# Performance work log

Hardware: AMD Instinct MI355X
Metric: run time of the kernel (lower is better)

Reference implementation:

```python
import jax, jax.numpy as jnp
import numpy as np

EPS = 1e-8
TEMP = 0.1
D, H = 512, 256  # hidden_dim, hidden_dim // 2
BI, R = 64, 36   # images, regions
BC, W = 64, 50   # captions, words


def _l2norm(x):
    n = jnp.linalg.norm(x, axis=-1, keepdims=True)
    return x / jnp.maximum(n, 1e-12)


def _gate(x, w1, b1, w2, b2):
    h = jax.nn.relu(x @ w1 + b1)
    return jax.nn.sigmoid(h @ w2 + b2)  # [..., 1]


def setup_inputs() -> dict:
    key = jax.random.key(0)
    ks = jax.random.split(key, 12)
    imgs = jax.random.normal(ks[0], (BI, R, D), dtype=jnp.float32)
    caps = jax.random.normal(ks[1], (BC, W, D), dtype=jnp.float32)
    img_lens = jax.random.randint(ks[2], (BI,), 1, R + 1).at[0].set(R).astype(jnp.int32)
    cap_lens = jax.random.randint(ks[3], (BC,), 1, W + 1).at[0].set(W).astype(jnp.int32)
    s = 0.02
    return {
        'imgs': imgs, 'caps': caps,
        'soft_w1': jax.random.normal(ks[4], (D, H), dtype=jnp.float32) * s,
        'soft_b1': jnp.zeros((H,), dtype=jnp.float32),
        'soft_w2': jax.random.normal(ks[5], (H, 1), dtype=jnp.float32) * s,
        'soft_b2': jnp.zeros((1,), dtype=jnp.float32),
        'hard_w1': jax.random.normal(ks[6], (D, H), dtype=jnp.float32) * s,
        'hard_b1': jnp.zeros((H,), dtype=jnp.float32),
        'hard_w2': jax.random.normal(ks[7], (H, 1), dtype=jnp.float32) * s,
        'hard_b2': jnp.zeros((1,), dtype=jnp.float32),
        'img_lens': img_lens, 'cap_lens': cap_lens,
    }


def reference(imgs, caps, soft_w1, soft_b1, soft_w2, soft_b2,
              hard_w1, hard_b1, hard_w2, hard_b2, img_lens, cap_lens):
    Bi, R_, D_ = imgs.shape
    Bc, W_, _ = caps.shape
    img_mask = jnp.arange(R_)[None, :] < img_lens[:, None]  # [Bi,R]
    cap_mask = jnp.arange(W_)[None, :] < cap_lens[:, None]  # [Bc,W]
    mask = img_mask[:, None, :, None] & cap_mask[None, :, None, :]  # [Bi,Bc,R,W]

    # fine-grained region-word similarities
    sims = jnp.einsum('ird,cwd->icrw', imgs, caps)

    # hard (top-1) attention: argmax over words, one-hot scatter, re-masked
    idx = jnp.argmax(jnp.where(mask, sims, -1.0), axis=-1)  # [Bi,Bc,R]
    hard_attn = jnp.where(mask, jax.nn.one_hot(idx, W_, dtype=sims.dtype), 0.0)

    # soft attention with temperature and mask
    soft = jax.nn.softmax(jnp.where(mask, sims / TEMP, -jnp.inf), axis=-1)
    soft_attn = jnp.where(mask, soft, 0.0)

    hard_wc = jnp.einsum('icrw,cwd->icrd', hard_attn, caps)
    soft_wc = jnp.einsum('icrw,cwd->icrd', soft_attn, caps)

    # per-region learned gates, normalized to sum ~1
    sg = _gate(imgs, soft_w1, soft_b1, soft_w2, soft_b2)  # [Bi,R,1]
    hg = _gate(imgs, hard_w1, hard_b1, hard_w2, hard_b2)  # [Bi,R,1]
    tot = sg + hg + EPS
    sg = (sg / tot)[:, None, :, :]  # [Bi,1,R,1]
    hg = (hg / tot)[:, None, :, :]

    mixed = sg * soft_wc + hg * hard_wc  # [Bi,Bc,R,D]

    # per-pair, per-region cosine similarity
    out = jnp.einsum('ird,icrd->icr', _l2norm(imgs), _l2norm(mixed))
    return jnp.where(img_mask[:, None, :], out, -1.0)  # [Bi,Bc,R]
```

## Files before the change

kernel.cpp:

```cpp
#include <hip/hip_runtime.h>
#include <math.h>

#define BI 64
#define RR 36
#define BC 64
#define WW 50
#define DD 512
#define HH 256
#define CST 132

typedef _Float16 f16x8 __attribute__((ext_vector_type(8)));
typedef _Float16 f16x4 __attribute__((ext_vector_type(4)));
typedef float    f32x4 __attribute__((ext_vector_type(4)));
typedef float    f32x16 __attribute__((ext_vector_type(16)));

__device__ __forceinline__ float wave_sum(float v){
  #pragma unroll
  for (int off=32; off>0; off>>=1) v += __shfl_xor(v, off, 64);
  return v;
}
__device__ __forceinline__ float wave_max(float v){
  #pragma unroll
  for (int off=32; off>0; off>>=1) v = fmaxf(v, __shfl_xor(v, off, 64));
  return v;
}

__device__ __forceinline__ void gl_lds16(const _Float16* g, _Float16* l){
  __builtin_amdgcn_global_load_lds(
      (const __attribute__((address_space(1))) unsigned int*)g,
      (__attribute__((address_space(3))) unsigned int*)l, 16, 0, 0);
}

__global__ __launch_bounds__(256) void prepgram_kernel(
    const float* __restrict__ imgs, const float* __restrict__ caps,
    const float* __restrict__ sw1, const float* __restrict__ hw1,
    _Float16* __restrict__ Ah, _Float16* __restrict__ Al,
    _Float16* __restrict__ Bh, _Float16* __restrict__ Bl,
    float* __restrict__ G, _Float16* __restrict__ Gfrag)
{
  __shared__ __align__(16) float smem[64*64];
  if (blockIdx.x < 1504){
    int u = blockIdx.x*256 + threadIdx.x;
    _Float16 *dh, *dl; int idx;
    if (u < 144*1024){ idx = u;            dh = Ah; dl = Al; }
    else             { idx = u - 144*1024; dh = Bh; dl = Bl; }
    const int tile = idx >> 10, rem = idx & 1023, ks = rem >> 6, lane = rem & 63;
    const int k0 = ks*32 + (lane >> 4)*8;
    f16x8 hv, lv;
    if (u < 144*1024 || tile < 200){
      const float* src = (u < 144*1024) ? imgs : caps;
      const int m = tile*16 + (lane & 15);
      const float* p = src + (size_t)m*DD + k0;
      #pragma unroll
      for (int j=0;j<8;j++){
        float a = p[j];
        _Float16 h = (_Float16)a;
        hv[j] = h;
        lv[j] = (_Float16)((a - (float)h) * 2048.0f);
      }
    } else {
      const int n = (tile-200)*16 + (lane & 15);
      const float* src = (n < HH) ? (sw1 + n) : (hw1 + n - HH);
      #pragma unroll
      for (int j=0;j<8;j++){
        float a = src[(size_t)(k0+j)*HH];
        _Float16 h = (_Float16)a;
        hv[j] = h;
        lv[j] = (_Float16)((a - (float)h) * 2048.0f);
      }
    }
    *(f16x8*)(dh + (size_t)idx*8) = hv;
    *(f16x8*)(dl + (size_t)idx*8) = lv;
  } else {
    float* Gt = smem;
    const int c = blockIdx.x - 1504;
    const int t = threadIdx.x, lane = t & 63, wv = t >> 6;
    const int wm = wv & 1, wn = wv >> 1;
    const float* cbase = caps + (size_t)c*WW*DD;

    f32x16 P, Q;
    #pragma unroll
    for (int e=0;e<16;e++){ P[e]=0.f; Q[e]=0.f; }

    const int r  = lane & 31;
    const int k8 = (lane >> 5)*8;
    const int wA = wm*32 + r;
    const int wB = wn*32 + r;
    const float* pA = cbase + (size_t)wA*DD + k8;
    const float* pB = cbase + (size_t)wB*DD + k8;

    for (int ks=0; ks<32; ks++){
      const int k0 = ks*16;
      float4 a0, a1, b0, b1;
      if (wA < WW){ a0 = *(const float4*)(pA + k0); a1 = *(const float4*)(pA + k0 + 4); }
      else        { a0 = (float4){0,0,0,0}; a1 = a0; }
      if (wB < WW){ b0 = *(const float4*)(pB + k0); b1 = *(const float4*)(pB + k0 + 4); }
      else        { b0 = (float4){0,0,0,0}; b1 = b0; }
      float av[8] = {a0.x,a0.y,a0.z,a0.w,a1.x,a1.y,a1.z,a1.w};
      float bw[8] = {b0.x,b0.y,b0.z,b0.w,b1.x,b1.y,b1.z,b1.w};
      f16x8 ah, al, bh, bl;
      #pragma unroll
      for (int j=0;j<8;j++){
        _Float16 h = (_Float16)av[j];
        ah[j] = h; al[j] = (_Float16)((av[j]-(float)h)*2048.0f);
        _Float16 g = (_Float16)bw[j];
        bh[j] = g; bl[j] = (_Float16)((bw[j]-(float)g)*2048.0f);
      }
      P = __builtin_amdgcn_mfma_f32_32x32x16_f16(ah, bh, P,0,0,0);
      Q = __builtin_amdgcn_mfma_f32_32x32x16_f16(ah, bl, Q,0,0,0);
      Q = __builtin_amdgcn_mfma_f32_32x32x16_f16(al, bh, Q,0,0,0);
    }

    const int col = wn*32 + (lane & 31);
    #pragma unroll
    for (int reg=0; reg<16; reg++){
      const int row = wm*32 + (reg&3) + 8*(reg>>2) + 4*(lane>>5);
      float g = P[reg] + Q[reg]*(1.0f/2048.0f);
      Gt[row*64 + col] = g;
      if (row < WW && col < WW)
        G[(size_t)c*WW*WW + row*WW + col] = g;
    }
    __syncthreads();

    #pragma unroll
    for (int tile=0; tile<4; tile++){
      int flat = t*4;
      int ks2 = flat>>9, L=(flat>>3)&63, j0=flat&7;
      const bool ones = (tile==3) && ((L&15)==2);
      int n  = tile*16 + (L&15);
      int kk = ks2*32 + ((L>>4)<<3) + j0;
      f16x4 v;
      #pragma unroll
      for (int e=0;e<4;e++)
        v[e] = ones ? (_Float16)1.0f : (_Float16)Gt[n*64 + kk + e];
      *(f16x4*)&Gfrag[(size_t)c*4096 + (tile*2+ks2)*512 + L*8 + j0] = v;
    }
  }
}

__global__ __launch_bounds__(256, 2) void sgemm_hgate_kernel(
    const _Float16* __restrict__ Ah, const _Float16* __restrict__ Al,
    const _Float16* __restrict__ Bh, const _Float16* __restrict__ Bl,
    float* __restrict__ Sp,
    const float* __restrict__ imgs,
    const float* __restrict__ sb1, const float* __restrict__ hb1,
    const float* __restrict__ sw2, const float* __restrict__ hw2,
    float* __restrict__ drawS, float* __restrict__ drawH,
    float* __restrict__ rnraw)
{
  __shared__ _Float16 lds[2*16384];
  const int t = threadIdx.x, lane = t & 63, wv = t >> 6;

  if (blockIdx.x >= 36){
    const int sg  = blockIdx.x - 36;
    const int xcd = sg & 7, sidx = sg >> 3;
    const int l   = (xcd < 2 ? xcd*57 : 114 + (xcd-2)*56) + sidx;
    const int st  = l / 45, wi = l - st*45;
    const int mbg = st & 1, nbg = st >> 1;
    const int mb  = mbg*9 + wi/5;
    const int nb  = nbg*5 + wi%5;
    const int wm = wv & 1, wn = wv >> 1;

    f32x4 P[4][4], Q[4][4];
    #pragma unroll
    for (int a=0;a<4;a++)
      #pragma unroll
      for (int b=0;b<4;b++){ P[a][b]=(f32x4){0,0,0,0}; Q[a][b]=(f32x4){0,0,0,0}; }

    const _Float16* sbase = (wv==0)?Ah:(wv==1)?Al:(wv==2)?Bh:Bl;
    const size_t gtb = (size_t)((wv<2)? mb : nb)*8;
    _Float16* buf0 = lds + wv*4096;
    _Float16* buf1 = lds + 16384 + wv*4096;

    #pragma unroll
    for (int s=0;s<8;s++)
      gl_lds16(sbase + (((gtb+s)*16 + 0)*64 + lane)*8, buf0 + s*512);
    asm volatile("s_waitcnt vmcnt(0)" ::: "memory");
    __syncthreads();

    for (int ks=0; ks<16; ks++){
      if (ks < 15){
        _Float16* nb_ = ((ks+1) & 1) ? buf1 : buf0;
        #pragma unroll
        for (int s=0;s<8;s++)
          gl_lds16(sbase + (((gtb+s)*16 + (ks+1))*64 + lane)*8, nb_ + s*512);
      }

      const _Float16* L = lds + (ks & 1)*16384;
      f16x8 a_h[4], a_l[4], b_h[4], b_l[4];
      #pragma unroll
      for (int x=0;x<4;x++){
        a_h[x] = *(const f16x8*)&L[        (wm*4+x)*512 + lane*8];
        a_l[x] = *(const f16x8*)&L[ 4096 + (wm*4+x)*512 + lane*8];
        b_h[x] = *(const f16x8*)&L[ 8192 + (wn*4+x)*512 + lane*8];
        b_l[x] = *(const f16x8*)&L[12288 + (wn*4+x)*512 + lane*8];
      }
      #pragma unroll
      for (int mi=0;mi<4;mi++)
        #pragma unroll
        for (int ni=0;ni<4;ni++){
          P[mi][ni] = __builtin_amdgcn_mfma_f32_16x16x32_f16(a_h[mi], b_h[ni], P[mi][ni],0,0,0);
          Q[mi][ni] = __builtin_amdgcn_mfma_f32_16x16x32_f16(a_h[mi], b_l[ni], Q[mi][ni],0,0,0);
          Q[mi][ni] = __builtin_amdgcn_mfma_f32_16x16x32_f16(a_l[mi], b_h[ni], Q[mi][ni],0,0,0);
        }

      if (ks < 15)
        asm volatile("s_waitcnt vmcnt(0)" ::: "memory");
      __syncthreads();
    }

    const int r0 = mb*128 + wm*64 + ((lane>>4)<<2);
    const int c0 = nb*128 + wn*64 + (lane&15);
    size_t pr[16]; size_t pc[4];
    #pragma unroll
    for (int mi=0;mi<4;mi++)
      #pragma unroll
      for (int reg=0;reg<4;reg++){
        unsigned row = (unsigned)(r0 + mi*16 + reg);
        unsigned i = row / 36u, rr_ = row - i*36u;
        pr[mi*4+reg] = (size_t)i*115200u + (size_t)rr_*50u;
      }
    #pragma unroll
    for (int ni=0;ni<4;ni++){
      unsigned col = (unsigned)(c0 + ni*16);
      unsigned cc = col / 50u, w = col - cc*50u;
      pc[ni] = (size_t)cc*1800u + w;
    }
    #pragma unroll
    for (int mi=0;mi<4;mi++)
      #pragma unroll
      for (int ni=0;ni<4;ni++)
        #pragma unroll
        for (int reg=0;reg<4;reg++)
          Sp[pr[mi*4+reg] + pc[ni]] =
              P[mi][ni][reg] + Q[mi][ni][reg]*(1.0f/2048.0f);
    return;
  }

  const int mb = blockIdx.x >> 1;
  const int br = blockIdx.x & 1;
  const int wm = wv & 1, wn = wv >> 1;

  f32x4 P[4][8];
  #pragma unroll
  for (int a=0;a<4;a++)
    #pragma unroll
    for (int b=0;b<8;b++) P[a][b]=(f32x4){0,0,0,0};

  const _Float16* Bbase = Bh + (size_t)(200 + br*16)*8192;

  #pragma unroll
  for (int s=0;s<6;s++){
    const int u = wv*6 + s;
    const _Float16* src = (u < 8)
      ? (Ah    + ((size_t)((mb*8 + u)*16 + 0)*64 + lane)*8)
      : (Bbase + ((size_t)((u-8)  *16 + 0)*64 + lane)*8);
    _Float16* dst = (u < 8) ? (lds + u*512) : (lds + 4096 + (u-8)*512);
    gl_lds16(src, dst);
  }
  asm volatile("s_waitcnt vmcnt(0)" ::: "memory");
  __syncthreads();

  for (int ks=0; ks<16; ks++){
    if (ks < 15){
      _Float16* buf = lds + (((ks+1) & 1) ? 16384 : 0);
      #pragma unroll
      for (int s=0;s<6;s++){
        const int u = wv*6 + s;
        const _Float16* src = (u < 8)
          ? (Ah    + ((size_t)((mb*8 + u)*16 + (ks+1))*64 + lane)*8)
          : (Bbase + ((size_t)((u-8)  *16 + (ks+1))*64 + lane)*8);
        _Float16* dst = (u < 8) ? (buf + u*512) : (buf + 4096 + (u-8)*512);
        gl_lds16(src, dst);
      }
    }

    const _Float16* L = lds + (ks & 1)*16384;
    f16x8 a[4], b[8];
    #pragma unroll
    for (int x=0;x<4;x++)
      a[x] = *(const f16x8*)&L[(wm*4+x)*512 + lane*8];
    #pragma unroll
    for (int y=0;y<8;y++)
      b[y] = *(const f16x8*)&L[4096 + (wn*8+y)*512 + lane*8];
    #pragma unroll
    for (int mi=0;mi<4;mi++)
      #pragma unroll
      for (int ni=0;ni<8;ni++)
        P[mi][ni] = __builtin_amdgcn_mfma_f32_16x16x32_f16(a[mi], b[ni], P[mi][ni],0,0,0);

    if (ks < 15)
      asm volatile("s_waitcnt vmcnt(0)" ::: "memory");
    __syncthreads();
  }

  const float* b1 = br ? hb1 : sb1;
  const float* w2 = br ? hw2 : sw2;
  float bvv[8], wvv[8];
  #pragma unroll
  for (int ni=0;ni<8;ni++){
    const int cb = wn*128 + ni*16 + (lane&15);
    bvv[ni] = b1[cb]; wvv[ni] = w2[cb];
  }
  float contrib[16];
  #pragma unroll
  for (int mi=0;mi<4;mi++)
    #pragma unroll
    for (int reg=0;reg<4;reg++){
      float cacc = 0.f;
      #pragma unroll
      for (int ni=0;ni<8;ni++)
        cacc = fmaf(fmaxf(P[mi][ni][reg] + bvv[ni], 0.f), wvv[ni], cacc);
      #pragma unroll
      for (int off=1; off<16; off<<=1) cacc += __shfl_xor(cacc, off, 64);
      contrib[mi*4+reg] = cacc;
    }

  float* red = (float*)lds;
  if ((lane & 15) == 0){
    const int rbase = wm*64 + ((lane>>4)<<2);
    #pragma unroll
    for (int mi=0;mi<4;mi++)
      #pragma unroll
      for (int reg=0;reg<4;reg++)
        red[wn*128 + rbase + mi*16 + reg] = contrib[mi*4+reg];
  }
  __syncthreads();
  if (t < 128){
    float draw = red[t] + red[128 + t];
    (br ? drawH : drawS)[mb*128 + t] = draw;
  }

  if (br == 0){
    const int row = mb*128 + (t >> 1);
    const float* p = imgs + (size_t)row*DD + (t & 1)*256;
    float ss = 0.f;
    #pragma unroll
    for (int q=0;q<64;q++){
      float4 x = ((const float4*)p)[q];
      ss += x.x*x.x + x.y*x.y + x.z*x.z + x.w*x.w;
    }
    ss += __shfl_xor(ss, 1, 64);
    if ((t & 1) == 0) rnraw[row] = ss;
  }
}

__global__ __launch_bounds__(256) void epi_kernel(
    const float* __restrict__ Sp,
    const int* __restrict__ img_lens, const int* __restrict__ cap_lens,
    const float* __restrict__ drawS, const float* __restrict__ drawH,
    const float* __restrict__ rnraw,
    const float* __restrict__ G, const _Float16* __restrict__ Gfrag,
    const float* __restrict__ sb2, const float* __restrict__ hb2,
    float* __restrict__ out)
{
  __shared__ __align__(16) _Float16 FT[4][48*72];
  const int t = threadIdx.x, lane = t & 63;
  const int wv = __builtin_amdgcn_readfirstlane(t >> 6);
  const int pair = blockIdx.x*4 + wv;
  const int i = pair >> 6, c = pair & 63;
  const int l = lane & 15, g = lane >> 4;
  const int cap_len = cap_lens[c];
  const int img_len = img_lens[i];

  int4 gf[8];
  #pragma unroll
  for (int q=0;q<8;q++)
    gf[q] = ((const int4*)(Gfrag + (size_t)c*4096))[q*64 + lane];

  const float* sbp = Sp + (size_t)i*115200 + (size_t)c*1800;
  float sv[3][16];
  #pragma unroll
  for (int nt=0;nt<3;nt++)
    #pragma unroll
    for (int ks=0;ks<2;ks++){
      const float* p = sbp + (nt*16+l)*50 + ks*32 + g*8;
      #pragma unroll
      for (int h=0;h<4;h++){
        float2 v2 = *(const float2*)(p + h*2);
        sv[nt][ks*8 + h*2]     = v2.x;
        sv[nt][ks*8 + h*2 + 1] = v2.y;
      }
    }

  float avA[3]; int aiA[3]; float denA[3], tSA[3];
  f16x8 e16[3][2];
  #pragma unroll
  for (int nt=0;nt<3;nt++){
    float best = -INFINITY; int bw = 64;
    #pragma unroll
    for (int j=0;j<16;j++){
      int w = (j>>3)*32 + g*8 + (j&7);
      if (w < cap_len){
        float s = sv[nt][j];
        if (s > best){ best = s; bw = w; }
      }
    }
    #pragma unroll
    for (int off=16; off<64; off<<=1){
      float ov = __shfl_xor(best, off, 64);
      int   ow = __shfl_xor(bw,   off, 64);
      if (ov > best || (ov == best && ow < bw)){ best = ov; bw = ow; }
    }
    avA[nt] = best; aiA[nt] = (bw < 64) ? bw : 0;

    float dsum = 0.f, tsum = 0.f;
    #pragma unroll
    for (int ks=0;ks<2;ks++)
      #pragma unroll
      for (int j=0;j<8;j++){
        int w = ks*32 + g*8 + j;
        float s = sv[nt][ks*8+j];
        float e = (w < cap_len) ? __expf(10.0f*(s - best)) : 0.f;
        _Float16 eh = (_Float16)e;
        e16[nt][ks][j] = eh;
        dsum += (float)eh;
        tsum += (float)(_Float16)(e * s);
      }
    dsum += __shfl_xor(dsum,16,64); dsum += __shfl_xor(dsum,32,64);
    tsum += __shfl_xor(tsum,16,64); tsum += __shfl_xor(tsum,32,64);
    denA[nt] = dsum; tSA[nt] = tsum;
  }

  _Float16* ft = &FT[wv][0];
  #pragma unroll
  for (int mt=0;mt<4;mt++)
    #pragma unroll
    for (int nt=0;nt<3;nt++){
      f32x4 acc = (f32x4){0,0,0,0};
      #pragma unroll
      for (int ks=0;ks<2;ks++){
        f16x8 ga = *(const f16x8*)&gf[mt*2+ks];
        acc = __builtin_amdgcn_mfma_f32_16x16x32_f16(ga, e16[nt][ks], acc,0,0,0);
      }
      f16x4 fv;
      #pragma unroll
      for (int r2=0;r2<4;r2++) fv[r2] = (_Float16)acc[r2];
      *(f16x4*)&ft[(nt*16+l)*72 + mt*16 + g*4] = fv;
    }

  float tQA[3];
  #pragma unroll
  for (int nt=0;nt<3;nt++){
    float q = 0.f;
    #pragma unroll
    for (int ks=0;ks<2;ks++){
      f16x8 fv = *(const f16x8*)&ft[(nt*16+l)*72 + ks*32 + g*8];
      #pragma unroll
      for (int j=0;j<8;j++)
        q += (float)e16[nt][ks][j] * (float)fv[j];
    }
    q += __shfl_xor(q,16,64); q += __shfl_xor(q,32,64);
    tQA[nt] = q;
  }

  if (lane < 16){
    const float sb2v = sb2[0], hb2v = hb2[0];
    #pragma unroll
    for (int nt=0;nt<3;nt++){
      const int rr = nt*16 + lane;
      if (rr < RR){
        const int ai = aiA[nt];
        const float av = avA[nt];
        float dh = (float)ft[rr*72 + ai];
        float hh = G[(size_t)c*WW*WW + ai*(WW+1)];
        float hv = (av > -1.0f) ? 1.f : 0.f;
        const int rg = i*RR + rr;
        float sg_ = 1.f/(1.f+__expf(-(drawS[rg] + sb2v)));
        float hg_ = 1.f/(1.f+__expf(-(drawH[rg] + hb2v)));
        float tot = sg_ + hg_ + 1e-8f;
        float gs = sg_/tot, gh = hg_/tot;
        float rx = 1.f/fmaxf(sqrtf(rnraw[rg]), 1e-12f);
        float dn = (float)(_Float16)denA[nt];
        float rd = 1.f/dn;
        float num = gs*(tSA[nt]*rd) + hv*gh*av;
        float n2  = gs*gs*(tQA[nt]*rd*rd) + hv*(2.f*gs*gh*(dh*rd) + gh*gh*hh);
        float ov  = num * rx / fmaxf(sqrtf(fmaxf(n2, 0.f)), 1e-12f);
        out[((size_t)i*BC + c)*RR + rr] = (rr < img_len) ? ov : -1.0f;
      }
    }
  }
}

__global__ __launch_bounds__(256) void gates_kernel(
    const float* __restrict__ imgs,
    const float* __restrict__ sw1, const float* __restrict__ sb1,
    const float* __restrict__ sw2, const float* __restrict__ sb2,
    const float* __restrict__ hw1, const float* __restrict__ hb1,
    const float* __restrict__ hw2, const float* __restrict__ hb2,
    float* __restrict__ sgn, float* __restrict__ hgn, float* __restrict__ rn)
{
  __shared__ __align__(16) float xs[8*DD];
  __shared__ float red[16*256];
  __shared__ float nr[8];
  const int t = threadIdx.x;
  const int row0 = blockIdx.x * 8;
  if (t < 8) nr[t] = 0.f;
  __syncthreads();
  const float4* src = (const float4*)(imgs + (size_t)row0*DD);
  #pragma unroll
  for (int m=0;m<4;m++){
    int n = m*256+t;
    float4 v = src[n];
    ((float4*)xs)[n] = v;
    float ss = v.x*v.x+v.y*v.y+v.z*v.z+v.w*v.w;
    atomicAdd(&nr[n>>7], ss);
  }
  __syncthreads();
  float accS[8]={0,0,0,0,0,0,0,0};
  float accH[8]={0,0,0,0,0,0,0,0};
  for (int k=0;k<DD;k+=4){
    float a0=sw1[(k+0)*HH+t], a1=sw1[(k+1)*HH+t], a2=sw1[(k+2)*HH+t], a3=sw1[(k+3)*HH+t];
    float b0=hw1[(k+0)*HH+t], b1=hw1[(k+1)*HH+t], b2=hw1[(k+2)*HH+t], b3=hw1[(k+3)*HH+t];
    #pragma unroll
    for (int r=0;r<8;r++){
      float4 x = *(const float4*)&xs[r*DD+k];
      accS[r]=fmaf(x.x,a0,accS[r]); accS[r]=fmaf(x.y,a1,accS[r]);
      accS[r]=fmaf(x.z,a2,accS[r]); accS[r]=fmaf(x.w,a3,accS[r]);
      accH[r]=fmaf(x.x,b0,accH[r]); accH[r]=fmaf(x.y,b1,accH[r]);
      accH[r]=fmaf(x.z,b2,accH[r]); accH[r]=fmaf(x.w,b3,accH[r]);
    }
  }
  const float b1s=sb1[t], b1h=hb1[t], w2s=sw2[t], w2h=hw2[t];
  #pragma unroll
  for (int r=0;r<8;r++){
    red[r*256+t]     = w2s * fmaxf(accS[r]+b1s, 0.f);
    red[(8+r)*256+t] = w2h * fmaxf(accH[r]+b1h, 0.f);
  }
  __syncthreads();
  const int wv=t>>6, ln=t&63;
  #pragma unroll
  for (int q=0;q<4;q++){
    int rr_ = wv*4+q;
    float v = red[rr_*256+ln]+red[rr_*256+ln+64]+red[rr_*256+ln+128]+red[rr_*256+ln+192];
    v = wave_sum(v);
    if (ln==0) red[rr_*256] = v;
  }
  __syncthreads();
  if (t<8){
    float os = red[t*256] + sb2[0];
    float oh = red[(8+t)*256] + hb2[0];
    float s = 1.f/(1.f+__expf(-os));
    float h = 1.f/(1.f+__expf(-oh));
    float tot = s+h+1e-8f;
    sgn[row0+t] = s/tot;
    hgn[row0+t] = h/tot;
    rn[row0+t]  = 1.f/fmaxf(sqrtf(nr[t]), 1e-12f);
  }
}

__global__ __launch_bounds__(256) void gram_fb_kernel(
    const float* __restrict__ caps, float* __restrict__ G)
{
  __shared__ __align__(16) float cs[WW*CST];
  const int c    = blockIdx.x >> 2;
  const int tile = blockIdx.x & 3;
  const int w0   = tile*13;
  const int nw   = (tile==3) ? 11 : 13;
  const int t=threadIdx.x, lane=t&63, wv=t>>6;
  const int wl = lane < WW ? lane : WW-1;
  float acc[4]={0.f,0.f,0.f,0.f};
  for (int k0=0;k0<DD;k0+=128){
    __syncthreads();
    for (int n=t;n<WW*32;n+=256){
      int row=n>>5, c4=(n&31)*4;
      *(float4*)&cs[row*CST+c4] = *(const float4*)(caps + ((size_t)c*WW+row)*DD + k0 + c4);
    }
    __syncthreads();
    for (int k=0;k<128;k+=4){
      float4 cv = *(const float4*)&cs[wl*CST+k];
      #pragma unroll
      for (int q=0;q<4;q++){
        int lw = wv + q*4;
        if (lw < nw){
          float4 bv = *(const float4*)&cs[(w0+lw)*CST+k];
          acc[q]=fmaf(bv.x,cv.x,acc[q]); acc[q]=fmaf(bv.y,cv.y,acc[q]);
          acc[q]=fmaf(bv.z,cv.z,acc[q]); acc[q]=fmaf(bv.w,cv.w,acc[q]);
        }
      }
    }
  }
  if (lane < WW){
    #pragma unroll
    for (int q=0;q<4;q++){
      int lw = wv + q*4;
      if (lw < nw) G[(size_t)c*WW*WW + (w0+lw)*WW + lane] = acc[q];
    }
  }
}

__global__ __launch_bounds__(256) void pair_kernel(
    const float* __restrict__ imgs, const float* __restrict__ caps,
    const int* __restrict__ img_lens, const int* __restrict__ cap_lens,
    const float* __restrict__ sgn, const float* __restrict__ hgn,
    const float* __restrict__ rn,
    const float* __restrict__ G, float* __restrict__ out)
{
  __shared__ __align__(16) float smem[WW*CST + 52*52 + RR*52];
  float* cs = smem;
  float* Gs = smem + WW*CST;
  float* As = Gs + 52*52;
  const int bx = blockIdx.x;
  const int i = bx >> 6, c = bx & 63;
  const int t = threadIdx.x, lane = t&63;
  const int wv = __builtin_amdgcn_readfirstlane(t>>6);
  const int wl = lane < WW ? lane : WW-1;
  const int cap_len = cap_lens[c];
  const int img_len = img_lens[i];
  for (int n=t;n<52*52;n+=256){
    int w=n/52, w2=n-w*52;
    Gs[n] = (w<WW && w2<WW) ? G[(size_t)c*WW*WW + w*WW + w2] : 0.f;
  }
  float acc[9]={0,0,0,0,0,0,0,0,0};
  const float* ib = imgs + ((size_t)i*RR + wv*9)*DD;
  for (int k0=0;k0<DD;k0+=128){
    __syncthreads();
    for (int n=t;n<WW*32;n+=256){
      int row=n>>5, c4=(n&31)*4;
      *(float4*)&cs[row*CST+c4] = *(const float4*)(caps + ((size_t)c*WW+row)*DD + k0 + c4);
    }
    __syncthreads();
    for (int k=0;k<128;k+=4){
      float4 cv = *(const float4*)&cs[wl*CST+k];
      #pragma unroll
      for (int j=0;j<9;j++){
        float4 iv = *(const float4*)(ib + j*DD + k0 + k);
        acc[j]=fmaf(iv.x,cv.x,acc[j]); acc[j]=fmaf(iv.y,cv.y,acc[j]);
        acc[j]=fmaf(iv.z,cv.z,acc[j]); acc[j]=fmaf(iv.w,cv.w,acc[j]);
      }
    }
  }
  for (int j=0;j<9;j++){
    const int r = wv*9 + j;
    const float s = acc[j];
    float av; int ai;
    if (lane < cap_len){ av = s;     ai = lane; }
    else if (lane < WW){ av = -1.0f; ai = lane; }
    else               { av = -INFINITY; ai = 64; }
    #pragma unroll
    for (int off=32; off>0; off>>=1){
      float ov = __shfl_xor(av, off, 64);
      int   oi = __shfl_xor(ai, off, 64);
      if (ov > av || (ov == av && oi < ai)){ av = ov; ai = oi; }
    }
    float zv = (lane < cap_len) ? s*10.0f : -INFINITY;
    float zm = wave_max(zv);
    float e  = (lane < cap_len) ? __expf(zv - zm) : 0.f;
    float den = wave_sum(e);
    if (lane < 52) As[r*52 + lane] = (lane < WW) ? e : 0.f;
    float m = 0.f;
    #pragma unroll
    for (int g=0; g<13; g++){
      float4 ab = *(const float4*)&As[r*52 + g*4];
      m = fmaf(ab.x, Gs[(g*4+0)*52+wl], m);
      m = fmaf(ab.y, Gs[(g*4+1)*52+wl], m);
      m = fmaf(ab.z, Gs[(g*4+2)*52+wl], m);
      m = fmaf(ab.w, Gs[(g*4+3)*52+wl], m);
    }
    float tS = wave_sum(e * s);
    float tQ = wave_sum(e * m);
    float dh = __shfl(m, ai, 64);
    float hh = Gs[ai*52 + ai];
    float hv = (ai < cap_len) ? 1.f : 0.f;
    const int rg = i*RR + r;
    float gs = sgn[rg], gh = hgn[rg], rx = rn[rg];
    float rd = 1.f/den;
    float num = gs*(tS*rd) + hv*gh*av;
    float n2  = gs*gs*(tQ*rd*rd) + hv*(2.f*gs*gh*(dh*rd) + gh*gh*hh);
    float ov  = num * rx / fmaxf(sqrtf(fmaxf(n2, 0.f)), 1e-12f);
    if (lane==0) out[((size_t)i*BC + c)*RR + r] = (r < img_len) ? ov : -1.0f;
  }
}

extern "C" void kernel_launch(void* const* d_in, const int* in_sizes, int n_in,
                              void* d_out, int out_size, void* d_ws, size_t ws_size,
                              hipStream_t stream)
{
  const float* imgs = (const float*)d_in[0];
  const float* caps = (const float*)d_in[1];
  const float* sw1  = (const float*)d_in[2];
  const float* sb1  = (const float*)d_in[3];
  const float* sw2  = (const float*)d_in[4];
  const float* sb2  = (const float*)d_in[5];
  const float* hw1  = (const float*)d_in[6];
  const float* hb1  = (const float*)d_in[7];
  const float* hw2  = (const float*)d_in[8];
  const float* hb2  = (const float*)d_in[9];
  const int* img_lens = (const int*)d_in[10];
  const int* cap_lens = (const int*)d_in[11];

  char* base = (char*)d_ws;
  float*    drawS = (float*)(base + 0);
  float*    drawH = (float*)(base + 9216);
  float*    rnraw = (float*)(base + 18432);
  float*    G     = (float*)(base + 27648);
  _Float16* Gfrag = (_Float16*)(base + 667648);
  _Float16* Ah    = (_Float16*)(base + 1191936);
  _Float16* Al    = (_Float16*)(base + 3551232);
  _Float16* Bh    = (_Float16*)(base + 5910528);
  _Float16* Bl    = (_Float16*)(base + 9711616);
  float*    Sp    = (float*)(base + 18231296);
  const size_t NEED = 47726592ull;

  float* out = (float*)d_out;

  if (ws_size >= NEED){
    hipLaunchKernelGGL(prepgram_kernel, dim3(1568), dim3(256), 0, stream,
                       imgs, caps, sw1, hw1, Ah, Al, Bh, Bl, G, Gfrag);
    hipLaunchKernelGGL(sgemm_hgate_kernel, dim3(486), dim3(256), 0, stream,
                       Ah, Al, Bh, Bl, Sp,
                       imgs, sb1, hb1, sw2, hw2, drawS, drawH, rnraw);
    hipLaunchKernelGGL(epi_kernel, dim3(1024), dim3(256), 0, stream,
                       Sp, img_lens, cap_lens, drawS, drawH, rnraw,
                       G, Gfrag, sb2, hb2, out);
  } else {
    hipLaunchKernelGGL(gates_kernel, dim3(288), dim3(256), 0, stream,
                       imgs, sw1, sb1, sw2, sb2, hw1, hb1, hw2, hb2,
                       drawS, drawH, rnraw);
    hipLaunchKernelGGL(gram_fb_kernel, dim3(256), dim3(256), 0, stream, caps, G);
    hipLaunchKernelGGL(pair_kernel, dim3(BI*BC), dim3(256), 0, stream,
                       imgs, caps, img_lens, cap_lens, drawS, drawH, rnraw, G, out);
  }
}
```

Measured before the change: 142.7 us.

## Fuse fp16 split conversion into GEMM kernels, dropping the prep pass

The separate prep kernel that split fp32 inputs and weights into hi/lo fp16 fragment buffers is removed. The similarity GEMM and gate GEMM blocks now load fp32 directly from global memory into registers, convert to hi/lo fp16 and write them to LDS in a register-staged double buffer. The caption Gram computation moves into the same launch as extra blocks. This removes one kernel launch and the round-trip of the fp16 fragment buffers through global memory, at the cost of more global bytes per tile (fp32 instead of fp16), repeated conversion work across tiles that share inputs, and strided uncoalesced weight loads in the gate path.

```diff
diff --git a/kernel.cpp b/kernel.cpp
--- a/kernel.cpp
+++ b/kernel.cpp
@@ -25,56 +25,128 @@
   return v;
 }
 
-__device__ __forceinline__ void gl_lds16(const _Float16* g, _Float16* l){
-  __builtin_amdgcn_global_load_lds(
-      (const __attribute__((address_space(1))) unsigned int*)g,
-      (__attribute__((address_space(3))) unsigned int*)l, 16, 0, 0);
-}
-
-__global__ __launch_bounds__(256) void prepgram_kernel(
+__global__ __launch_bounds__(256, 2) void sgemm_hgate_kernel(
     const float* __restrict__ imgs, const float* __restrict__ caps,
     const float* __restrict__ sw1, const float* __restrict__ hw1,
-    _Float16* __restrict__ Ah, _Float16* __restrict__ Al,
-    _Float16* __restrict__ Bh, _Float16* __restrict__ Bl,
+    const float* __restrict__ sb1, const float* __restrict__ hb1,
+    const float* __restrict__ sw2, const float* __restrict__ hw2,
+    float* __restrict__ Sp,
+    float* __restrict__ drawS, float* __restrict__ drawH,
+    float* __restrict__ rnraw,
     float* __restrict__ G, _Float16* __restrict__ Gfrag)
 {
-  __shared__ __align__(16) float smem[64*64];
-  if (blockIdx.x < 1504){
-    int u = blockIdx.x*256 + threadIdx.x;
-    _Float16 *dh, *dl; int idx;
-    if (u < 144*1024){ idx = u;            dh = Ah; dl = Al; }
-    else             { idx = u - 144*1024; dh = Bh; dl = Bl; }
-    const int tile = idx >> 10, rem = idx & 1023, ks = rem >> 6, lane = rem & 63;
-    const int k0 = ks*32 + (lane >> 4)*8;
-    f16x8 hv, lv;
-    if (u < 144*1024 || tile < 200){
-      const float* src = (u < 144*1024) ? imgs : caps;
-      const int m = tile*16 + (lane & 15);
-      const float* p = src + (size_t)m*DD + k0;
-      #pragma unroll
-      for (int j=0;j<8;j++){
-        float a = p[j];
-        _Float16 h = (_Float16)a;
-        hv[j] = h;
-        lv[j] = (_Float16)((a - (float)h) * 2048.0f);
-      }
-    } else {
-      const int n = (tile-200)*16 + (lane & 15);
-      const float* src = (n < HH) ? (sw1 + n) : (hw1 + n - HH);
-      #pragma unroll
-      for (int j=0;j<8;j++){
-        float a = src[(size_t)(k0+j)*HH];
-        _Float16 h = (_Float16)a;
-        hv[j] = h;
-        lv[j] = (_Float16)((a - (float)h) * 2048.0f);
-      }
-    }
-    *(f16x8*)(dh + (size_t)idx*8) = hv;
-    *(f16x8*)(dl + (size_t)idx*8) = lv;
-  } else {
-    float* Gt = smem;
-    const int c = blockIdx.x - 1504;
-    const int t = threadIdx.x, lane = t & 63, wv = t >> 6;
+  __shared__ __align__(16) _Float16 lds[2*16384];
+  const int t = threadIdx.x, lane = t & 63, wv = t >> 6;
+
+  if (blockIdx.x >= 36 && blockIdx.x < 486){
+    const int sg  = blockIdx.x - 36;
+    const int xcd = sg & 7, sidx = sg >> 3;
+    const int l   = (xcd < 2 ? xcd*57 : 114 + (xcd-2)*56) + sidx;
+    const int st  = l / 45, wi = l - st*45;
+    const int mbg = st & 1, nbg = st >> 1;
+    const int mb  = mbg*9 + wi/5;
+    const int nb  = nbg*5 + wi%5;
+    const int wm = wv & 1, wn = wv >> 1;
+
+    f32x4 P[4][4], Q[4][4];
+    #pragma unroll
+    for (int a=0;a<4;a++)
+      #pragma unroll
+      for (int b=0;b<4;b++){ P[a][b]=(f32x4){0,0,0,0}; Q[a][b]=(f32x4){0,0,0,0}; }
+
+    const float* srcb = (wv < 2) ? imgs : caps;
+    const int tb   = ((wv<2)? mb : nb)*8 + (wv&1)*4;
+    const int mrow = lane & 15;
+    const int kq   = (lane >> 4)*8;
+    const float* sp0 = srcb + ((size_t)(tb*16 + mrow))*DD + kq;
+    const int regoff = ((wv<2)? 0 : 8192) + ((wv&1)*4)*512 + lane*8;
+
+    float4 va[4], vb[4];
+    auto sg_load = [&](int ks){
+      #pragma unroll
+      for (int s=0;s<4;s++){
+        const float* p = sp0 + (size_t)s*16*DD + ks*32;
+        va[s] = *(const float4*)p;
+        vb[s] = *(const float4*)(p+4);
+      }
+    };
+    auto sg_write = [&](int bufi){
+      _Float16* Lh = lds + bufi*16384 + regoff;
+      #pragma unroll
+      for (int s=0;s<4;s++){
+        float e[8] = {va[s].x,va[s].y,va[s].z,va[s].w,
+                      vb[s].x,vb[s].y,vb[s].z,vb[s].w};
+        f16x8 hv, lv;
+        #pragma unroll
+        for (int j=0;j<8;j++){
+          _Float16 h = (_Float16)e[j];
+          hv[j] = h;
+          lv[j] = (_Float16)((e[j]-(float)h)*2048.0f);
+        }
+        *(f16x8*)&Lh[s*512]        = hv;
+        *(f16x8*)&Lh[4096 + s*512] = lv;
+      }
+    };
+
+    sg_load(0); sg_write(0);
+    __syncthreads();
+
+    for (int ks=0; ks<16; ks++){
+      if (ks < 15) sg_load(ks+1);
+
+      const _Float16* L = lds + (ks & 1)*16384;
+      f16x8 a_h[4], a_l[4], b_h[4], b_l[4];
+      #pragma unroll
+      for (int x=0;x<4;x++){
+        a_h[x] = *(const f16x8*)&L[        (wm*4+x)*512 + lane*8];
+        a_l[x] = *(const f16x8*)&L[ 4096 + (wm*4+x)*512 + lane*8];
+        b_h[x] = *(const f16x8*)&L[ 8192 + (wn*4+x)*512 + lane*8];
+        b_l[x] = *(const f16x8*)&L[12288 + (wn*4+x)*512 + lane*8];
+      }
+      #pragma unroll
+      for (int mi=0;mi<4;mi++)
+        #pragma unroll
+        for (int ni=0;ni<4;ni++){
+          P[mi][ni] = __builtin_amdgcn_mfma_f32_16x16x32_f16(a_h[mi], b_h[ni], P[mi][ni],0,0,0);
+          Q[mi][ni] = __builtin_amdgcn_mfma_f32_16x16x32_f16(a_h[mi], b_l[ni], Q[mi][ni],0,0,0);
+          Q[mi][ni] = __builtin_amdgcn_mfma_f32_16x16x32_f16(a_l[mi], b_h[ni], Q[mi][ni],0,0,0);
+        }
+
+      if (ks < 15) sg_write((ks+1)&1);
+      __syncthreads();
+    }
+
+    const int r0 = mb*128 + wm*64 + ((lane>>4)<<2);
+    const int c0 = nb*128 + wn*64 + (lane&15);
+    size_t pr[16]; size_t pc[4];
+    #pragma unroll
+    for (int mi=0;mi<4;mi++)
+      #pragma unroll
+      for (int reg=0;reg<4;reg++){
+        unsigned row = (unsigned)(r0 + mi*16 + reg);
+        unsigned i = row / 36u, rr_ = row - i*36u;
+        pr[mi*4+reg] = (size_t)i*115200u + (size_t)rr_*50u;
+      }
+    #pragma unroll
+    for (int ni=0;ni<4;ni++){
+      unsigned col = (unsigned)(c0 + ni*16);
+      unsigned cc = col / 50u, w = col - cc*50u;
+      pc[ni] = (size_t)cc*1800u + w;
+    }
+    #pragma unroll
+    for (int mi=0;mi<4;mi++)
+      #pragma unroll
+      for (int ni=0;ni<4;ni++)
+        #pragma unroll
+        for (int reg=0;reg<4;reg++)
+          Sp[pr[mi*4+reg] + pc[ni]] =
+              P[mi][ni][reg] + Q[mi][ni][reg]*(1.0f/2048.0f);
+    return;
+  }
+
+  if (blockIdx.x >= 486){
+    float* Gt = (float*)lds;
+    const int c = blockIdx.x - 486;
     const int wm = wv & 1, wn = wv >> 1;
     const float* cbase = caps + (size_t)c*WW*DD;
 
@@ -135,111 +207,13 @@
         v[e] = ones ? (_Float16)1.0f : (_Float16)Gt[n*64 + kk + e];
       *(f16x4*)&Gfrag[(size_t)c*4096 + (tile*2+ks2)*512 + L*8 + j0] = v;
     }
-  }
-}
-
-__global__ __launch_bounds__(256, 2) void sgemm_hgate_kernel(
-    const _Float16* __restrict__ Ah, const _Float16* __restrict__ Al,
-    const _Float16* __restrict__ Bh, const _Float16* __restrict__ Bl,
-    float* __restrict__ Sp,
-    const float* __restrict__ imgs,
-    const float* __restrict__ sb1, const float* __restrict__ hb1,
-    const float* __restrict__ sw2, const float* __restrict__ hw2,
-    float* __restrict__ drawS, float* __restrict__ drawH,
-    float* __restrict__ rnraw)
-{
-  __shared__ _Float16 lds[2*16384];
-  const int t = threadIdx.x, lane = t & 63, wv = t >> 6;
-
-  if (blockIdx.x >= 36){
-    const int sg  = blockIdx.x - 36;
-    const int xcd = sg & 7, sidx = sg >> 3;
-    const int l   = (xcd < 2 ? xcd*57 : 114 + (xcd-2)*56) + sidx;
-    const int st  = l / 45, wi = l - st*45;
-    const int mbg = st & 1, nbg = st >> 1;
-    const int mb  = mbg*9 + wi/5;
-    const int nb  = nbg*5 + wi%5;
-    const int wm = wv & 1, wn = wv >> 1;
-
-    f32x4 P[4][4], Q[4][4];
-    #pragma unroll
-    for (int a=0;a<4;a++)
-      #pragma unroll
-      for (int b=0;b<4;b++){ P[a][b]=(f32x4){0,0,0,0}; Q[a][b]=(f32x4){0,0,0,0}; }
-
-    const _Float16* sbase = (wv==0)?Ah:(wv==1)?Al:(wv==2)?Bh:Bl;
-    const size_t gtb = (size_t)((wv<2)? mb : nb)*8;
-    _Float16* buf0 = lds + wv*4096;
-    _Float16* buf1 = lds + 16384 + wv*4096;
-
-    #pragma unroll
-    for (int s=0;s<8;s++)
-      gl_lds16(sbase + (((gtb+s)*16 + 0)*64 + lane)*8, buf0 + s*512);
-    asm volatile("s_waitcnt vmcnt(0)" ::: "memory");
-    __syncthreads();
-
-    for (int ks=0; ks<16; ks++){
-      if (ks < 15){
-        _Float16* nb_ = ((ks+1) & 1) ? buf1 : buf0;
-        #pragma unroll
-        for (int s=0;s<8;s++)
-          gl_lds16(sbase + (((gtb+s)*16 + (ks+1))*64 + lane)*8, nb_ + s*512);
-      }
-
-      const _Float16* L = lds + (ks & 1)*16384;
-      f16x8 a_h[4], a_l[4], b_h[4], b_l[4];
-      #pragma unroll
-      for (int x=0;x<4;x++){
-        a_h[x] = *(const f16x8*)&L[        (wm*4+x)*512 + lane*8];
-        a_l[x] = *(const f16x8*)&L[ 4096 + (wm*4+x)*512 + lane*8];
-        b_h[x] = *(const f16x8*)&L[ 8192 + (wn*4+x)*512 + lane*8];
-        b_l[x] = *(const f16x8*)&L[12288 + (wn*4+x)*512 + lane*8];
-      }
-      #pragma unroll
-      for (int mi=0;mi<4;mi++)
-        #pragma unroll
-        for (int ni=0;ni<4;ni++){
-          P[mi][ni] = __builtin_amdgcn_mfma_f32_16x16x32_f16(a_h[mi], b_h[ni], P[mi][ni],0,0,0);
-          Q[mi][ni] = __builtin_amdgcn_mfma_f32_16x16x32_f16(a_h[mi], b_l[ni], Q[mi][ni],0,0,0);
-          Q[mi][ni] = __builtin_amdgcn_mfma_f32_16x16x32_f16(a_l[mi], b_h[ni], Q[mi][ni],0,0,0);
-        }
-
-      if (ks < 15)
-        asm volatile("s_waitcnt vmcnt(0)" ::: "memory");
-      __syncthreads();
-    }
-
-    const int r0 = mb*128 + wm*64 + ((lane>>4)<<2);
-    const int c0 = nb*128 + wn*64 + (lane&15);
-    size_t pr[16]; size_t pc[4];
-    #pragma unroll
-    for (int mi=0;mi<4;mi++)
-      #pragma unroll
-      for (int reg=0;reg<4;reg++){
-        unsigned row = (unsigned)(r0 + mi*16 + reg);
-        unsigned i = row / 36u, rr_ = row - i*36u;
-        pr[mi*4+reg] = (size_t)i*115200u + (size_t)rr_*50u;
-      }
-    #pragma unroll
-    for (int ni=0;ni<4;ni++){
-      unsigned col = (unsigned)(c0 + ni*16);
-      unsigned cc = col / 50u, w = col - cc*50u;
-      pc[ni] = (size_t)cc*1800u + w;
-    }
-    #pragma unroll
-    for (int mi=0;mi<4;mi++)
-      #pragma unroll
-      for (int ni=0;ni<4;ni++)
-        #pragma unroll
-        for (int reg=0;reg<4;reg++)
-          Sp[pr[mi*4+reg] + pc[ni]] =
-              P[mi][ni][reg] + Q[mi][ni][reg]*(1.0f/2048.0f);
     return;
   }
 
   const int mb = blockIdx.x >> 1;
   const int br = blockIdx.x & 1;
   const int wm = wv & 1, wn = wv >> 1;
+  const float* W = br ? hw1 : sw1;
 
   f32x4 P[4][8];
   #pragma unroll
@@ -247,33 +221,51 @@
     #pragma unroll
     for (int b=0;b<8;b++) P[a][b]=(f32x4){0,0,0,0};
 
-  const _Float16* Bbase = Bh + (size_t)(200 + br*16)*8192;
-
-  #pragma unroll
-  for (int s=0;s<6;s++){
-    const int u = wv*6 + s;
-    const _Float16* src = (u < 8)
-      ? (Ah    + ((size_t)((mb*8 + u)*16 + 0)*64 + lane)*8)
-      : (Bbase + ((size_t)((u-8)  *16 + 0)*64 + lane)*8);
-    _Float16* dst = (u < 8) ? (lds + u*512) : (lds + 4096 + (u-8)*512);
-    gl_lds16(src, dst);
-  }
-  asm volatile("s_waitcnt vmcnt(0)" ::: "memory");
+  const int mrow = lane & 15, kq = (lane>>4)*8;
+  const float* apA = imgs + ((size_t)((mb*8 + wv*2)*16 + mrow))*DD + kq;
+  const int nb0 = (wv*4)*16 + mrow;
+
+  float4 va[2][2];
+  float wreg[4][8];
+  auto hg_load = [&](int ks){
+    #pragma unroll
+    for (int s=0;s<2;s++){
+      const float* p = apA + (size_t)s*16*DD + ks*32;
+      va[s][0] = *(const float4*)p;
+      va[s][1] = *(const float4*)(p+4);
+    }
+    #pragma unroll
+    for (int sb=0;sb<4;sb++){
+      const float* q = W + (size_t)(ks*32 + kq)*HH + (nb0 + sb*16);
+      #pragma unroll
+      for (int j=0;j<8;j++) wreg[sb][j] = q[(size_t)j*HH];
+    }
+  };
+  auto hg_write = [&](int bufi){
+    _Float16* buf = lds + bufi*16384;
+    #pragma unroll
+    for (int s=0;s<2;s++){
+      float e[8] = {va[s][0].x,va[s][0].y,va[s][0].z,va[s][0].w,
+                    va[s][1].x,va[s][1].y,va[s][1].z,va[s][1].w};
+      f16x8 hv;
+      #pragma unroll
+      for (int j=0;j<8;j++) hv[j] = (_Float16)e[j];
+      *(f16x8*)&buf[(wv*2+s)*512 + lane*8] = hv;
+    }
+    #pragma unroll
+    for (int sb=0;sb<4;sb++){
+      f16x8 hv;
+      #pragma unroll
+      for (int j=0;j<8;j++) hv[j] = (_Float16)wreg[sb][j];
+      *(f16x8*)&buf[4096 + (wv*4+sb)*512 + lane*8] = hv;
+    }
+  };
+
+  hg_load(0); hg_write(0);
   __syncthreads();
 
   for (int ks=0; ks<16; ks++){
-    if (ks < 15){
-      _Float16* buf = lds + (((ks+1) & 1) ? 16384 : 0);
-      #pragma unroll
-      for (int s=0;s<6;s++){
-        const int u = wv*6 + s;
-        const _Float16* src = (u < 8)
-          ? (Ah    + ((size_t)((mb*8 + u)*16 + (ks+1))*64 + lane)*8)
-          : (Bbase + ((size_t)((u-8)  *16 + (ks+1))*64 + lane)*8);
-        _Float16* dst = (u < 8) ? (buf + u*512) : (buf + 4096 + (u-8)*512);
-        gl_lds16(src, dst);
-      }
-    }
+    if (ks < 15) hg_load(ks+1);
 
     const _Float16* L = lds + (ks & 1)*16384;
     f16x8 a[4], b[8];
@@ -289,8 +281,7 @@
       for (int ni=0;ni<8;ni++)
         P[mi][ni] = __builtin_amdgcn_mfma_f32_16x16x32_f16(a[mi], b[ni], P[mi][ni],0,0,0);
 
-    if (ks < 15)
-      asm volatile("s_waitcnt vmcnt(0)" ::: "memory");
+    if (ks < 15) hg_write((ks+1)&1);
     __syncthreads();
   }
 
@@ -317,6 +308,7 @@
     }
 
   float* red = (float*)lds;
+  __syncthreads();
   if ((lane & 15) == 0){
     const int rbase = wm*64 + ((lane>>4)<<2);
     #pragma unroll
@@ -695,21 +687,15 @@
   float*    rnraw = (float*)(base + 18432);
   float*    G     = (float*)(base + 27648);
   _Float16* Gfrag = (_Float16*)(base + 667648);
-  _Float16* Ah    = (_Float16*)(base + 1191936);
-  _Float16* Al    = (_Float16*)(base + 3551232);
-  _Float16* Bh    = (_Float16*)(base + 5910528);
-  _Float16* Bl    = (_Float16*)(base + 9711616);
   float*    Sp    = (float*)(base + 18231296);
   const size_t NEED = 47726592ull;
 
   float* out = (float*)d_out;
 
   if (ws_size >= NEED){
-    hipLaunchKernelGGL(prepgram_kernel, dim3(1568), dim3(256), 0, stream,
-                       imgs, caps, sw1, hw1, Ah, Al, Bh, Bl, G, Gfrag);
-    hipLaunchKernelGGL(sgemm_hgate_kernel, dim3(486), dim3(256), 0, stream,
-                       Ah, Al, Bh, Bl, Sp,
-                       imgs, sb1, hb1, sw2, hw2, drawS, drawH, rnraw);
+    hipLaunchKernelGGL(sgemm_hgate_kernel, dim3(550), dim3(256), 0, stream,
+                       imgs, caps, sw1, hw1, sb1, hb1, sw2, hw2,
+                       Sp, drawS, drawH, rnraw, G, Gfrag);
     hipLaunchKernelGGL(epi_kernel, dim3(1024), dim3(256), 0, stream,
                        Sp, img_lens, cap_lens, drawS, drawH, rnraw,
                        G, Gfrag, sb2, hb2, out);
```

Result: no change. 143.6 us (+0.6%).
